# Optimization experiments

Measured on AMD Instinct MI355X. Metric: run time of the kernel, lower is better.

The kernel has to match this reference:

```python
import jax, jax.numpy as jnp
import numpy as np

B, N, D = 32, 1024, 3
Z_SCALES = jnp.array([2.0, 4.0, 8.0, 16.0, 32.0], dtype=jnp.float32)
Z_DIM = 16.0
BETA = 0.01          # kl_warmup done (epoch >= kl_warmup_epochs), so beta == args.beta
SINK_EPS = 0.1       # entropic regularization for the EMD (Sinkhorn) approximation
SINK_ITERS = 20
BIG = 1e8
NEG = -1e9


def _sqdist(x, y):
    # x: [B,N,D], y: [B,M,D] -> squared euclidean distances [B,N,M]
    xx = jnp.sum(x * x, -1)[:, :, None]
    yy = jnp.sum(y * y, -1)[:, None, :]
    xy = jnp.einsum('bnd,bmd->bnm', x, y)
    return jnp.maximum(xx + yy - 2.0 * xy, 0.0)


def _chamfer(x, xm, y, ym):
    # masked bidirectional chamfer: mean over valid points, mean over batch
    d = _sqdist(x, y)                                             # [B,N,M]
    d_xy = jnp.min(jnp.where(ym[:, None, :], d, BIG), axis=2)     # [B,N]
    d_yx = jnp.min(jnp.where(xm[:, :, None], d, BIG), axis=1)     # [B,M]
    nx = jnp.sum(xm, -1).astype(x.dtype)
    ny = jnp.sum(ym, -1).astype(x.dtype)
    cd = (jnp.sum(jnp.where(xm, d_xy, 0.0), -1) / nx
          + jnp.sum(jnp.where(ym, d_yx, 0.0), -1) / ny)
    return jnp.mean(cd)


def _emd_sinkhorn(x, xm, y, ym):
    # entropic-OT approximation of the masked EMD (log-domain Sinkhorn)
    C = _sqdist(x, y)                                             # [B,N,M]
    C = jnp.where(xm[:, :, None] & ym[:, None, :], C, BIG)
    nx = jnp.sum(xm, -1).astype(x.dtype)                          # [B]
    ny = jnp.sum(ym, -1).astype(x.dtype)
    log_a = jnp.where(xm, -jnp.log(nx)[:, None], NEG)             # [B,N]
    log_b = jnp.where(ym, -jnp.log(ny)[:, None], NEG)             # [B,M]

    @jax.checkpoint
    def step(carry, _):
        f, g = carry
        f = SINK_EPS * (log_a - jax.nn.logsumexp((g[:, None, :] - C) / SINK_EPS, axis=2))
        g = SINK_EPS * (log_b - jax.nn.logsumexp((f[:, :, None] - C) / SINK_EPS, axis=1))
        return (f, g), None

    f0 = jnp.zeros_like(log_a)
    g0 = jnp.zeros_like(log_b)
    (f, g), _ = jax.lax.scan(step, (f0, g0), None, length=SINK_ITERS)
    logP = (f[:, :, None] + g[:, None, :] - C) / SINK_EPS         # transport plan (log)
    emd = jnp.sum(jnp.exp(logP) * C, axis=(1, 2))                 # [B]
    return jnp.mean(emd)


def setup_inputs() -> dict:
    key = jax.random.key(0)
    k1, k2, k3 = jax.random.split(key, 3)
    return {
        'output_set': jax.random.normal(k1, (B, N, D), dtype=jnp.float32),
        'output_mask': jnp.ones((B, N), dtype=bool),
        'target_set': jax.random.normal(k2, (B, N, D), dtype=jnp.float32),
        'target_mask': jnp.ones((B, N), dtype=bool),
        'kls': jax.random.uniform(k3, (B, Z_SCALES.shape[0]), dtype=jnp.float32),
    }


def reference(output_set, output_mask, target_set, target_mask, kls):
    cd = _chamfer(output_set, output_mask, target_set, target_mask)
    emd = _emd_sinkhorn(output_set, output_mask, target_set, target_mask)
    recon_loss = cd + emd
    kl_loss = jnp.mean(jnp.sum(kls, axis=1))
    loss = BETA * kl_loss + recon_loss
    topdown_kl = jnp.mean(kls, axis=0) / (Z_SCALES * Z_DIM)        # [L]
    return loss, kl_loss, recon_loss, topdown_kl
```

## Files before the change

kernel.cpp:

```cpp
#include <hip/hip_runtime.h>
#include <math.h>

#define BB 32
#define NN 1024
#define NEGV (-1e9f)
#define BIGC (1e8f)
#define EPSS 0.1f
#define K2f   14.426950408889634f
#define TWOK2 28.853900817779268f
#define INVK2 0.06931471805599453f
#define SINK_ITERS 20
#define CHUNKS 16

__device__ __forceinline__ float wave_reduce_sum(float v) {
#pragma unroll
  for (int s = 32; s >= 1; s >>= 1) v += __shfl_xor(v, s, 64);
  return v;
}
__device__ __forceinline__ float wave_reduce_max(float v) {
#pragma unroll
  for (int s = 32; s >= 1; s >>= 1) v = fmaxf(v, __shfl_xor(v, s, 64));
  return v;
}
__device__ __forceinline__ float wave_reduce_min(float v) {
#pragma unroll
  for (int s = 32; s >= 1; s >>= 1) v = fminf(v, __shfl_xor(v, s, 64));
  return v;
}

__global__ __launch_bounds__(1024) void prep_kernel(
    const float* __restrict__ xset, const int* __restrict__ xm,
    const float* __restrict__ yset, const int* __restrict__ ym,
    float4* __restrict__ xpack, float4* __restrict__ ypack,
    float* __restrict__ elax, float* __restrict__ elay,
    float* __restrict__ invx, float* __restrict__ invy)
{
  const int b = blockIdx.x;
  const int n = threadIdx.x;
  const size_t idx = (size_t)b * NN + n;

  const float x0 = xset[idx * 3 + 0], x1 = xset[idx * 3 + 1], x2 = xset[idx * 3 + 2];
  const float y0 = yset[idx * 3 + 0], y1 = yset[idx * 3 + 1], y2 = yset[idx * 3 + 2];
  xpack[idx] = make_float4(x0, x1, x2, x0 * x0 + x1 * x1 + x2 * x2);
  ypack[idx] = make_float4(y0, y1, y2, y0 * y0 + y1 * y1 + y2 * y2);

  float cx = wave_reduce_sum(xm[idx] ? 1.0f : 0.0f);
  float cy = wave_reduce_sum(ym[idx] ? 1.0f : 0.0f);

  __shared__ float sx[16], sy[16];
  const int wave = n >> 6, lane = n & 63;
  if (lane == 0) { sx[wave] = cx; sy[wave] = cy; }
  __syncthreads();
  if (n == 0) {
    float a = 0.0f, c = 0.0f;
#pragma unroll
    for (int i = 0; i < 16; ++i) { a += sx[i]; c += sy[i]; }
    elax[b] = -EPSS * logf(a);
    elay[b] = -EPSS * logf(c);
    invx[b] = 1.0f / a;
    invy[b] = 1.0f / c;
  }
}

template<bool FIRST, bool CHAMF>
__global__ __launch_bounds__(512) void sink_step(
    const float4* __restrict__ rowpk, const float4* __restrict__ redpk,
    const int* __restrict__ rowmask, const int* __restrict__ redmask,
    const float* __restrict__ pot_in, float* __restrict__ pot_out,
    const float* __restrict__ ela,
    const float* __restrict__ invn,
    float* __restrict__ cd_part)
{
  const int b = blockIdx.y, chunk = blockIdx.x, tid = threadIdx.x;
  const int wave = tid >> 6, lane = tid & 63;
  const size_t base = (size_t)b * NN;

  __shared__ float4 ypk[NN];
  __shared__ float Aj[NN];
  __shared__ float reds[8];

  for (int i = tid; i < NN; i += 512) {
    const float4 yp = redpk[base + i];
    ypk[i] = yp;
    float a;
    if constexpr (FIRST)
      a = redmask[base + i] ? (-K2f * yp.w) : -1e30f;
    else
      a = redmask[base + i] ? fmaf(K2f, pot_in[base + i], -K2f * yp.w) : -1e30f;
    Aj[i] = a;
  }
  __syncthreads();

  const float elab = ela[b];
  float cdacc = 0.0f;

#pragma unroll 1
  for (int grp = 0; grp < 2; ++grp) {
    const int row0 = chunk * 64 + wave * 8 + grp * 4;

    float xs0[4], xs1[4], xs2[4], xw[4];
    int rmv[4];
#pragma unroll
    for (int r = 0; r < 4; ++r) {
      const float4 xp = rowpk[base + row0 + r];
      xs0[r] = TWOK2 * xp.x; xs1[r] = TWOK2 * xp.y; xs2[r] = TWOK2 * xp.z;
      xw[r] = xp.w;
      rmv[r] = rowmask[base + row0 + r];
    }

    float u[4][16];
#pragma unroll
    for (int j = 0; j < 16; ++j) {
      const int m = lane + j * 64;
      const float4 yp = ypk[m];
      const float aj = Aj[m];
#pragma unroll
      for (int r = 0; r < 4; ++r) {
        float t = fmaf(xs0[r], yp.x, aj);
        t = fmaf(xs1[r], yp.y, t);
        t = fmaf(xs2[r], yp.z, t);
        u[r][j] = t;
      }
    }

    float gm[4];
#pragma unroll
    for (int r = 0; r < 4; ++r) {
      const float a0 = fmaxf(fmaxf(u[r][0], u[r][1]), u[r][2]);
      const float a1 = fmaxf(fmaxf(u[r][3], u[r][4]), u[r][5]);
      const float a2 = fmaxf(fmaxf(u[r][6], u[r][7]), u[r][8]);
      const float a3 = fmaxf(fmaxf(u[r][9], u[r][10]), u[r][11]);
      const float a4 = fmaxf(fmaxf(u[r][12], u[r][13]), u[r][14]);
      const float mr = fmaxf(fmaxf(fmaxf(a0, a1), a2),
                             fmaxf(fmaxf(a3, a4), u[r][15]));
      gm[r] = wave_reduce_max(mr);
    }

    float ss[4] = {0.f, 0.f, 0.f, 0.f};
#pragma unroll
    for (int j = 0; j < 16; ++j) {
#pragma unroll
      for (int r = 0; r < 4; ++r)
        ss[r] += __builtin_amdgcn_exp2f(u[r][j] - gm[r]);
    }
#pragma unroll
    for (int r = 0; r < 4; ++r) ss[r] = wave_reduce_sum(ss[r]);

    if (lane == 0) {
#pragma unroll
      for (int r = 0; r < 4; ++r) {
        const float lse2 = gm[r] + __builtin_amdgcn_logf(ss[r]);
        const float el = rmv[r] ? elab : (EPSS * NEGV);
        pot_out[base + row0 + r] = el + xw[r] - INVK2 * lse2;
        if constexpr (CHAMF) {
          if (rmv[r])
            cdacc += fmaxf(fmaf(-INVK2, gm[r], xw[r]), 0.0f);
        }
      }
    }
  }

  if constexpr (CHAMF) {
    if (lane == 0) reds[wave] = cdacc;
    __syncthreads();
    if (tid == 0) {
      float s = 0.f;
#pragma unroll
      for (int w = 0; w < 8; ++w) s += reds[w];
      cd_part[(size_t)b * CHUNKS + chunk] = s * invn[b] * (1.0f / BB);
    }
  }
}

__global__ __launch_bounds__(512) void sink_fast(
    const float4* __restrict__ rowpk, const float4* __restrict__ redpk,
    const int* __restrict__ rowmask, const int* __restrict__ redmask,
    const float* __restrict__ pot_in, float* __restrict__ fpot,
    const float* __restrict__ ela)
{
  const int b = blockIdx.y, chunk = blockIdx.x, tid = threadIdx.x;
  const int wave = tid >> 6, lane = tid & 63;
  const size_t base = (size_t)b * NN;

  __shared__ float4 colq[NN];

  for (int i = tid; i < NN; i += 512) {
    const float4 yp = redpk[base + i];
    const float aj = redmask[base + i]
        ? fmaf(K2f, pot_in[base + i], -K2f * yp.w) : -1e30f;
    colq[i] = make_float4(yp.x, yp.y, yp.z, aj);
  }
  __syncthreads();

  const float elab = ela[b];
  const int row0 = chunk * 64 + wave * 8;

  float xs0[8], xs1[8], xs2[8], sh[8], acc[8], fp[8];
  int rmv[8];
#pragma unroll
  for (int r = 0; r < 8; ++r) {
    const float4 xp = rowpk[base + row0 + r];
    rmv[r] = rowmask[base + row0 + r];
    fp[r] = fpot[base + row0 + r];
    xs0[r] = TWOK2 * xp.x; xs1[r] = TWOK2 * xp.y; xs2[r] = TWOK2 * xp.z;
    sh[r] = rmv[r] ? (K2f * (elab + xp.w - fp[r])) : 3.0e38f;
    acc[r] = 0.0f;
  }

#pragma unroll 4
  for (int j = 0; j < 16; ++j) {
    const float4 q = colq[lane + j * 64];
#pragma unroll
    for (int r = 0; r < 8; ++r) {
      float t = fmaf(xs0[r], q.x, q.w);
      t = fmaf(xs1[r], q.y, t);
      t = fmaf(xs2[r], q.z, t);
      acc[r] += __builtin_amdgcn_exp2f(t - sh[r]);
    }
  }

#pragma unroll
  for (int r = 0; r < 8; ++r) acc[r] = wave_reduce_sum(acc[r]);

  if (lane == 0) {
#pragma unroll
    for (int r = 0; r < 8; ++r) {
      const float l2 = fminf(fmaxf(__builtin_amdgcn_logf(acc[r]), -120.0f), 120.0f);
      fpot[base + row0 + r] = rmv[r] ? (fp[r] - INVK2 * l2) : (EPSS * NEGV);
    }
  }
}

__global__ __launch_bounds__(512) void chamfer_dir(
    const float4* __restrict__ rowpk, const float4* __restrict__ redpk,
    const int* __restrict__ rowmask, const int* __restrict__ redmask,
    const float* __restrict__ invn, float* __restrict__ part)
{
  const int b = blockIdx.y, chunk = blockIdx.x, tid = threadIdx.x;
  const int wave = tid >> 6, lane = tid & 63;
  const size_t base = (size_t)b * NN;

  __shared__ float4 xw4[NN];
  for (int i = tid; i < NN; i += 512) {
    float4 xp = redpk[base + i];
    xp.w = redmask[base + i] ? xp.w : BIGC;
    xw4[i] = xp;
  }
  __syncthreads();

  float acc = 0.0f;
#pragma unroll 1
  for (int rr = 0; rr < 8; ++rr) {
    const int row = chunk * 64 + wave * 8 + rr;
    const float4 yp = rowpk[base + row];
    const float ys0 = -2.f * yp.x, ys1 = -2.f * yp.y, ys2 = -2.f * yp.z;
    float dmin = BIGC;
#pragma unroll
    for (int j = 0; j < 16; ++j) {
      const float4 xq = xw4[lane + j * 64];
      float d = fmaf(ys0, xq.x, xq.w);
      d = fmaf(ys1, xq.y, d);
      d = fmaf(ys2, xq.z, d);
      dmin = fminf(dmin, d);
    }
    dmin = wave_reduce_min(dmin);
    if (lane == 0 && rowmask[base + row]) acc += fmaxf(yp.w + dmin, 0.0f);
  }

  __shared__ float reds[8];
  if (lane == 0) reds[wave] = acc;
  __syncthreads();
  if (tid == 0) {
    float s = 0.f;
#pragma unroll
    for (int w = 0; w < 8; ++w) s += reds[w];
    part[(size_t)b * CHUNKS + chunk] = s * invn[b] * (1.0f / BB);
  }
}

__global__ __launch_bounds__(512) void emd_kernel(
    const float4* __restrict__ rowpk, const float4* __restrict__ redpk,
    const int* __restrict__ rowmask, const int* __restrict__ redmask,
    const float* __restrict__ frow, const float* __restrict__ gred,
    float* __restrict__ part)
{
  const int b = blockIdx.y, chunk = blockIdx.x, tid = threadIdx.x;
  const int wave = tid >> 6, lane = tid & 63;
  const size_t base = (size_t)b * NN;

  __shared__ float4 ypk[NN];
  __shared__ float Ag[NN];
  __shared__ float gv[NN];
  for (int i = tid; i < NN; i += 512) {
    const float4 yp = redpk[base + i];
    ypk[i] = yp;
    const float gg = gred[base + i];
    gv[i] = gg;
    Ag[i] = redmask[base + i] ? fmaf(K2f, gg, -K2f * yp.w) : -1e30f;
  }
  __syncthreads();

  float acc = 0.0f;
#pragma unroll 1
  for (int rr = 0; rr < 8; ++rr) {
    const int row = chunk * 64 + wave * 8 + rr;
    const float4 xp = rowpk[base + row];
    const float fv = frow[base + row];
    const float rc = fmaf(K2f, fv, -K2f * xp.w);
    const float xs0 = TWOK2 * xp.x, xs1 = TWOK2 * xp.y, xs2 = TWOK2 * xp.z;
    const bool rv = rowmask[base + row] != 0;
#pragma unroll
    for (int j = 0; j < 16; ++j) {
      const int m = lane + j * 64;
      const float4 yp = ypk[m];
      const float a = rv ? (Ag[m] + rc) : -1e30f;
      float t = fmaf(xs0, yp.x, a);
      t = fmaf(xs1, yp.y, t);
      t = fmaf(xs2, yp.z, t);
      float C = fmaf(t, -INVK2, fv + gv[m]);
      C = fmaxf(C, 0.0f);
      acc = fmaf(__builtin_amdgcn_exp2f(t), C, acc);
    }
  }

  acc = wave_reduce_sum(acc);
  __shared__ float reds[8];
  if (lane == 0) reds[wave] = acc;
  __syncthreads();
  if (tid == 0) {
    float s = 0.f;
#pragma unroll
    for (int w = 0; w < 8; ++w) s += reds[w];
    part[(size_t)b * CHUNKS + chunk] = s * (1.0f / BB);
  }
}

__global__ __launch_bounds__(256) void final_kernel(
    const float* __restrict__ cd_part, const float* __restrict__ emd_part,
    const float* __restrict__ kls, float* __restrict__ out)
{
  const int tid = threadIdx.x, wave = tid >> 6, lane = tid & 63;
  __shared__ float sh[12];
  float s1 = 0.f, s2 = 0.f, s3 = 0.f;
  for (int i = tid; i < 2 * BB * CHUNKS; i += 256) s1 += cd_part[i];
  for (int i = tid; i < BB * CHUNKS; i += 256) s2 += emd_part[i];
  for (int i = tid; i < BB * 5; i += 256) s3 += kls[i];
  s1 = wave_reduce_sum(s1); s2 = wave_reduce_sum(s2); s3 = wave_reduce_sum(s3);
  if (lane == 0) { sh[wave] = s1; sh[4 + wave] = s2; sh[8 + wave] = s3; }
  __syncthreads();
  if (tid == 0) {
    const float cd = sh[0] + sh[1] + sh[2] + sh[3];
    const float emd = sh[4] + sh[5] + sh[6] + sh[7];
    const float kl = (sh[8] + sh[9] + sh[10] + sh[11]) / (float)BB;
    out[0] = 0.01f * kl + (cd + emd);
    out[1] = kl;
    out[2] = cd + emd;
  }
  if (tid < 5) {
    float cs = 0.f;
    for (int b2 = 0; b2 < BB; ++b2) cs += kls[b2 * 5 + tid];
    const float zs[5] = {2.f, 4.f, 8.f, 16.f, 32.f};
    out[3 + tid] = (cs / (float)BB) / (zs[tid] * 16.f);
  }
}

extern "C" void kernel_launch(void* const* d_in, const int* in_sizes, int n_in,
                              void* d_out, int out_size, void* d_ws, size_t ws_size,
                              hipStream_t stream)
{
  const float* xset = (const float*)d_in[0];
  const int*   xm   = (const int*)d_in[1];
  const float* yset = (const float*)d_in[2];
  const int*   ym   = (const int*)d_in[3];
  const float* kls  = (const float*)d_in[4];

  float* ws = (float*)d_ws;
  float*  f    = ws;
  float*  g    = f + BB * NN;
  float4* xp4  = (float4*)(g + BB * NN);
  float4* yp4  = xp4 + BB * NN;
  float*  elax = (float*)(yp4 + BB * NN);
  float*  elay = elax + BB;
  float*  invx = elay + BB;
  float*  invy = invx + BB;
  float*  cd   = invy + BB;
  float*  emdp = cd + 2 * BB * CHUNKS;

  prep_kernel<<<dim3(BB), 1024, 0, stream>>>(xset, xm, yset, ym,
                                             xp4, yp4, elax, elay, invx, invy);

  const dim3 sg(CHUNKS, BB);
  sink_step<true, true><<<sg, 512, 0, stream>>>(xp4, yp4, xm, ym, nullptr, f,
                                                elax, invx, cd);
  chamfer_dir<<<sg, 512, 0, stream>>>(yp4, xp4, ym, xm, invy, cd + BB * CHUNKS);
  sink_step<false, false><<<sg, 512, 0, stream>>>(yp4, xp4, ym, xm, f, g,
                                                  elay, nullptr, nullptr);
  for (int it = 1; it < SINK_ITERS; ++it) {
    sink_fast<<<sg, 512, 0, stream>>>(xp4, yp4, xm, ym, g, f, elax);
    sink_fast<<<sg, 512, 0, stream>>>(yp4, xp4, ym, xm, f, g, elay);
  }

  emd_kernel<<<sg, 512, 0, stream>>>(xp4, yp4, xm, ym, f, g, emdp);
  final_kernel<<<1, 256, 0, stream>>>(cd, emdp, kls, (float*)d_out);
}
```

Measured before the change: 444.2 us.

## Fuse Sinkhorn iterations into one cooperative kernel with per-batch barriers

Replaces the chain of about 43 kernel launches (prep, chamfer, 40 Sinkhorn half-steps, EMD) with one cooperative persistent kernel of 512 blocks. Each batch's 16 blocks sync through an atomic counter barrier, and point data stays in LDS for the whole run instead of being reloaded on every launch. This removes launch overhead and the repeated global loads of packed points. The cost is spin-wait barriers, a large LDS footprint per block, and reliance on all blocks being co-resident, with a fallback to the old kernel chain if the cooperative launch fails.

```diff
diff --git a/kernel.cpp b/kernel.cpp
--- a/kernel.cpp
+++ b/kernel.cpp
@@ -11,6 +11,7 @@
 #define INVK2 0.06931471805599453f
 #define SINK_ITERS 20
 #define CHUNKS 16
+#define NBLK (BB * CHUNKS)
 
 __device__ __forceinline__ float wave_reduce_sum(float v) {
 #pragma unroll
@@ -26,6 +27,319 @@
 #pragma unroll
   for (int s = 32; s >= 1; s >>= 1) v = fminf(v, __shfl_xor(v, s, 64));
   return v;
+}
+
+__device__ __forceinline__ bool getbit(const unsigned* mb, int i) {
+  return (mb[i >> 5] >> (i & 31)) & 1u;
+}
+
+__device__ __forceinline__ float pot_ld(const float* p) {
+  return __hip_atomic_load(p, __ATOMIC_RELAXED, __HIP_MEMORY_SCOPE_AGENT);
+}
+__device__ __forceinline__ void pot_st(float* p, float v) {
+  __hip_atomic_store(p, v, __ATOMIC_RELAXED, __HIP_MEMORY_SCOPE_AGENT);
+}
+
+__device__ __forceinline__ void batch_barrier(int* bar, int b, int gen, int tid) {
+  __syncthreads();
+  if (tid == 0) {
+    __hip_atomic_fetch_add(&bar[b], 1, __ATOMIC_RELEASE, __HIP_MEMORY_SCOPE_AGENT);
+    const int target = CHUNKS * gen;
+    while (__hip_atomic_load(&bar[b], __ATOMIC_RELAXED, __HIP_MEMORY_SCOPE_AGENT) < target)
+      __builtin_amdgcn_s_sleep(2);
+    (void)__hip_atomic_load(&bar[b], __ATOMIC_ACQUIRE, __HIP_MEMORY_SCOPE_AGENT);
+  }
+  __syncthreads();
+}
+
+template<bool CHAMF>
+__device__ __forceinline__ void twopass(
+    const float4* rl, const float4* cl, const float* Agl, const unsigned* rmb,
+    float elab, int c, int wave, int lane, int tid,
+    float* __restrict__ potOut, size_t base,
+    float invnb, int b, float* __restrict__ cdPart, float* reds)
+{
+  float cdacc = 0.0f;
+#pragma unroll 1
+  for (int grp = 0; grp < 2; ++grp) {
+    const int row0 = c * 64 + wave * 8 + grp * 4;
+
+    float xs0[4], xs1[4], xs2[4], xw[4];
+    bool rmv[4];
+#pragma unroll
+    for (int r = 0; r < 4; ++r) {
+      const float4 xp = rl[row0 + r];
+      xs0[r] = TWOK2 * xp.x; xs1[r] = TWOK2 * xp.y; xs2[r] = TWOK2 * xp.z;
+      xw[r] = xp.w;
+      rmv[r] = getbit(rmb, row0 + r);
+    }
+
+    float u[4][16];
+#pragma unroll
+    for (int j = 0; j < 16; ++j) {
+      const int m = lane + j * 64;
+      const float4 yp = cl[m];
+      const float aj = Agl[m];
+#pragma unroll
+      for (int r = 0; r < 4; ++r) {
+        float t = fmaf(xs0[r], yp.x, aj);
+        t = fmaf(xs1[r], yp.y, t);
+        t = fmaf(xs2[r], yp.z, t);
+        u[r][j] = t;
+      }
+    }
+
+    float gm[4];
+#pragma unroll
+    for (int r = 0; r < 4; ++r) {
+      const float a0 = fmaxf(fmaxf(u[r][0], u[r][1]), u[r][2]);
+      const float a1 = fmaxf(fmaxf(u[r][3], u[r][4]), u[r][5]);
+      const float a2 = fmaxf(fmaxf(u[r][6], u[r][7]), u[r][8]);
+      const float a3 = fmaxf(fmaxf(u[r][9], u[r][10]), u[r][11]);
+      const float a4 = fmaxf(fmaxf(u[r][12], u[r][13]), u[r][14]);
+      const float mr = fmaxf(fmaxf(fmaxf(a0, a1), a2),
+                             fmaxf(fmaxf(a3, a4), u[r][15]));
+      gm[r] = wave_reduce_max(mr);
+    }
+
+    float ss[4] = {0.f, 0.f, 0.f, 0.f};
+#pragma unroll
+    for (int j = 0; j < 16; ++j) {
+#pragma unroll
+      for (int r = 0; r < 4; ++r)
+        ss[r] += __builtin_amdgcn_exp2f(u[r][j] - gm[r]);
+    }
+#pragma unroll
+    for (int r = 0; r < 4; ++r) ss[r] = wave_reduce_sum(ss[r]);
+
+#pragma unroll
+    for (int r = 0; r < 4; ++r) {
+      const float lse2 = gm[r] + __builtin_amdgcn_logf(ss[r]);
+      const float el = rmv[r] ? elab : (EPSS * NEGV);
+      const float pv = el + xw[r] - INVK2 * lse2;
+      if (lane == 0) {
+        pot_st(&potOut[base + row0 + r], pv);
+        if constexpr (CHAMF) {
+          if (rmv[r]) cdacc += fmaxf(fmaf(-INVK2, gm[r], xw[r]), 0.0f);
+        }
+      }
+    }
+  }
+
+  if constexpr (CHAMF) {
+    if (lane == 0) reds[wave] = cdacc;
+    __syncthreads();
+    if (tid == 0) {
+      float s = 0.f;
+#pragma unroll
+      for (int w = 0; w < 8; ++w) s += reds[w];
+      cdPart[(size_t)b * CHUNKS + c] = s * invnb * (1.0f / BB);
+    }
+  }
+}
+
+__device__ __forceinline__ void onepass(
+    const float4* rl, const float4* cl, const float* Agl, const unsigned* rmb,
+    float elab, int row0, int lane, float* __restrict__ pot, size_t base)
+{
+  float xs0[8], xs1[8], xs2[8], sh[8], acc[8], fp[8];
+  bool rmv[8];
+#pragma unroll
+  for (int r = 0; r < 8; ++r) {
+    const float4 xp = rl[row0 + r];
+    rmv[r] = getbit(rmb, row0 + r);
+    fp[r] = pot_ld(&pot[base + row0 + r]);
+    xs0[r] = TWOK2 * xp.x; xs1[r] = TWOK2 * xp.y; xs2[r] = TWOK2 * xp.z;
+    sh[r] = rmv[r] ? (K2f * (elab + xp.w - fp[r])) : 3.0e38f;
+    acc[r] = 0.0f;
+  }
+
+#pragma unroll 4
+  for (int j = 0; j < 16; ++j) {
+    const int m = lane + j * 64;
+    const float4 q = cl[m];
+    const float aj = Agl[m];
+#pragma unroll
+    for (int r = 0; r < 8; ++r) {
+      float t = fmaf(xs0[r], q.x, aj);
+      t = fmaf(xs1[r], q.y, t);
+      t = fmaf(xs2[r], q.z, t);
+      acc[r] += __builtin_amdgcn_exp2f(t - sh[r]);
+    }
+  }
+
+#pragma unroll
+  for (int r = 0; r < 8; ++r) acc[r] = wave_reduce_sum(acc[r]);
+
+  if (lane == 0) {
+#pragma unroll
+    for (int r = 0; r < 8; ++r) {
+      const float l2 = fminf(fmaxf(__builtin_amdgcn_logf(acc[r]), -120.0f), 120.0f);
+      pot_st(&pot[base + row0 + r], rmv[r] ? (fp[r] - INVK2 * l2) : (EPSS * NEGV));
+    }
+  }
+}
+
+__global__ __launch_bounds__(512, 4) void fused_sink(
+    const float* __restrict__ xset, const int* __restrict__ xm,
+    const float* __restrict__ yset, const int* __restrict__ ym,
+    float* __restrict__ f, float* __restrict__ g,
+    float* __restrict__ cd_part, float* __restrict__ emd_part,
+    int* __restrict__ bar)
+{
+  const int gid = blockIdx.x;
+  const int b = gid & (BB - 1), c = gid >> 5;
+  const int tid = threadIdx.x, wave = tid >> 6, lane = tid & 63;
+  const size_t base = (size_t)b * NN;
+
+  __shared__ float4 xl[NN];
+  __shared__ float4 yl[NN];
+  __shared__ float Ag[NN];
+  __shared__ float gvs[NN];
+  __shared__ unsigned xmb[NN / 32], ymb[NN / 32];
+  __shared__ float cred[16];
+  __shared__ float reds[8];
+  __shared__ float sscal[4];
+
+  float cntx = 0.f, cnty = 0.f;
+  for (int i = tid; i < NN; i += 512) {
+    const size_t ix = (base + (size_t)i) * 3;
+    const float x0 = xset[ix], x1 = xset[ix + 1], x2 = xset[ix + 2];
+    const float y0 = yset[ix], y1 = yset[ix + 1], y2 = yset[ix + 2];
+    xl[i] = make_float4(x0, x1, x2, x0 * x0 + x1 * x1 + x2 * x2);
+    yl[i] = make_float4(y0, y1, y2, y0 * y0 + y1 * y1 + y2 * y2);
+    const int mxv = xm[base + i], myv = ym[base + i];
+    cntx += mxv ? 1.0f : 0.0f;
+    cnty += myv ? 1.0f : 0.0f;
+    const unsigned long long bx = __ballot(mxv != 0);
+    const unsigned long long by = __ballot(myv != 0);
+    if (lane == 0) {
+      const int w0 = i >> 5;
+      xmb[w0] = (unsigned)bx; xmb[w0 + 1] = (unsigned)(bx >> 32);
+      ymb[w0] = (unsigned)by; ymb[w0 + 1] = (unsigned)(by >> 32);
+    }
+  }
+  cntx = wave_reduce_sum(cntx);
+  cnty = wave_reduce_sum(cnty);
+  if (lane == 0) { cred[wave] = cntx; cred[8 + wave] = cnty; }
+  __syncthreads();
+  if (tid == 0) {
+    float a = 0.f, cc = 0.f;
+#pragma unroll
+    for (int i = 0; i < 8; ++i) { a += cred[i]; cc += cred[8 + i]; }
+    sscal[0] = -EPSS * logf(a);
+    sscal[1] = -EPSS * logf(cc);
+    sscal[2] = 1.0f / a;
+    sscal[3] = 1.0f / cc;
+  }
+  __syncthreads();
+  const float elax = sscal[0], elay = sscal[1], invx = sscal[2], invy = sscal[3];
+  int gen = 0;
+
+  for (int i = tid; i < NN; i += 512)
+    Ag[i] = getbit(ymb, i) ? (-K2f * yl[i].w) : -1e30f;
+  __syncthreads();
+  twopass<true>(xl, yl, Ag, xmb, elax, c, wave, lane, tid, f, base,
+                invx, b, cd_part, reds);
+
+  for (int i = tid; i < NN; i += 512)
+    gvs[i] = getbit(xmb, i) ? xl[i].w : BIGC;
+  __syncthreads();
+  {
+    float acc = 0.0f;
+#pragma unroll 1
+    for (int rr = 0; rr < 8; ++rr) {
+      const int row = c * 64 + wave * 8 + rr;
+      const float4 yp = yl[row];
+      const float ys0 = -2.f * yp.x, ys1 = -2.f * yp.y, ys2 = -2.f * yp.z;
+      float dmin = BIGC;
+#pragma unroll
+      for (int j = 0; j < 16; ++j) {
+        const int m = lane + j * 64;
+        const float4 xq = xl[m];
+        float d = fmaf(ys0, xq.x, gvs[m]);
+        d = fmaf(ys1, xq.y, d);
+        d = fmaf(ys2, xq.z, d);
+        dmin = fminf(dmin, d);
+      }
+      dmin = wave_reduce_min(dmin);
+      if (lane == 0 && getbit(ymb, row)) acc += fmaxf(yp.w + dmin, 0.0f);
+    }
+    __syncthreads();
+    if (lane == 0) reds[wave] = acc;
+    __syncthreads();
+    if (tid == 0) {
+      float s = 0.f;
+#pragma unroll
+      for (int w = 0; w < 8; ++w) s += reds[w];
+      cd_part[BB * CHUNKS + (size_t)b * CHUNKS + c] = s * invy * (1.0f / BB);
+    }
+  }
+
+  batch_barrier(bar, b, ++gen, tid);
+
+  for (int i = tid; i < NN; i += 512)
+    Ag[i] = getbit(xmb, i) ? fmaf(K2f, pot_ld(&f[base + i]), -K2f * xl[i].w) : -1e30f;
+  __syncthreads();
+  twopass<false>(yl, xl, Ag, ymb, elay, c, wave, lane, tid, g, base,
+                 0.f, b, nullptr, reds);
+
+  batch_barrier(bar, b, ++gen, tid);
+
+  for (int it = 1; it < SINK_ITERS; ++it) {
+    for (int i = tid; i < NN; i += 512)
+      Ag[i] = getbit(ymb, i) ? fmaf(K2f, pot_ld(&g[base + i]), -K2f * yl[i].w) : -1e30f;
+    __syncthreads();
+    onepass(xl, yl, Ag, xmb, elax, c * 64 + wave * 8, lane, f, base);
+    batch_barrier(bar, b, ++gen, tid);
+
+    for (int i = tid; i < NN; i += 512)
+      Ag[i] = getbit(xmb, i) ? fmaf(K2f, pot_ld(&f[base + i]), -K2f * xl[i].w) : -1e30f;
+    __syncthreads();
+    onepass(yl, xl, Ag, ymb, elay, c * 64 + wave * 8, lane, g, base);
+    batch_barrier(bar, b, ++gen, tid);
+  }
+
+  for (int i = tid; i < NN; i += 512) {
+    const float gg = pot_ld(&g[base + i]);
+    gvs[i] = gg;
+    Ag[i] = getbit(ymb, i) ? fmaf(K2f, gg, -K2f * yl[i].w) : -1e30f;
+  }
+  __syncthreads();
+  {
+    float acc = 0.0f;
+#pragma unroll 1
+    for (int rr = 0; rr < 8; ++rr) {
+      const int row = c * 64 + wave * 8 + rr;
+      const float4 xp = xl[row];
+      const float fv = pot_ld(&f[base + row]);
+      const float rc = fmaf(K2f, fv, -K2f * xp.w);
+      const float xs0 = TWOK2 * xp.x, xs1 = TWOK2 * xp.y, xs2 = TWOK2 * xp.z;
+      const bool rv = getbit(xmb, row);
+#pragma unroll
+      for (int j = 0; j < 16; ++j) {
+        const int m = lane + j * 64;
+        const float4 yp = yl[m];
+        const float a = rv ? (Ag[m] + rc) : -1e30f;
+        float t = fmaf(xs0, yp.x, a);
+        t = fmaf(xs1, yp.y, t);
+        t = fmaf(xs2, yp.z, t);
+        float C = fmaf(t, -INVK2, fv + gvs[m]);
+        C = fmaxf(C, 0.0f);
+        acc = fmaf(__builtin_amdgcn_exp2f(t), C, acc);
+      }
+    }
+    acc = wave_reduce_sum(acc);
+    __syncthreads();
+    if (lane == 0) reds[wave] = acc;
+    __syncthreads();
+    if (tid == 0) {
+      float s = 0.f;
+#pragma unroll
+      for (int w = 0; w < 8; ++w) s += reds[w];
+      emd_part[(size_t)b * CHUNKS + c] = s * (1.0f / BB);
+    }
+  }
 }
 
 __global__ __launch_bounds__(1024) void prep_kernel(
@@ -377,29 +691,38 @@
   float* ws = (float*)d_ws;
   float*  f    = ws;
   float*  g    = f + BB * NN;
-  float4* xp4  = (float4*)(g + BB * NN);
-  float4* yp4  = xp4 + BB * NN;
-  float*  elax = (float*)(yp4 + BB * NN);
+  float*  cd   = g + BB * NN;
+  float*  emdp = cd + 2 * BB * CHUNKS;
+  float*  elax = emdp + BB * CHUNKS;
   float*  elay = elax + BB;
   float*  invx = elay + BB;
   float*  invy = invx + BB;
-  float*  cd   = invy + BB;
-  float*  emdp = cd + 2 * BB * CHUNKS;
-
-  prep_kernel<<<dim3(BB), 1024, 0, stream>>>(xset, xm, yset, ym,
-                                             xp4, yp4, elax, elay, invx, invy);
-
-  const dim3 sg(CHUNKS, BB);
-  sink_step<true, true><<<sg, 512, 0, stream>>>(xp4, yp4, xm, ym, nullptr, f,
-                                                elax, invx, cd);
-  chamfer_dir<<<sg, 512, 0, stream>>>(yp4, xp4, ym, xm, invy, cd + BB * CHUNKS);
-  sink_step<false, false><<<sg, 512, 0, stream>>>(yp4, xp4, ym, xm, f, g,
-                                                  elay, nullptr, nullptr);
-  for (int it = 1; it < SINK_ITERS; ++it) {
-    sink_fast<<<sg, 512, 0, stream>>>(xp4, yp4, xm, ym, g, f, elax);
-    sink_fast<<<sg, 512, 0, stream>>>(yp4, xp4, ym, xm, f, g, elay);
-  }
-
-  emd_kernel<<<sg, 512, 0, stream>>>(xp4, yp4, xm, ym, f, g, emdp);
+  int*    bar  = (int*)(invy + BB);
+  float4* xp4  = (float4*)(ws + 67232);
+  float4* yp4  = xp4 + BB * NN;
+
+  hipMemsetAsync(bar, 0, BB * sizeof(int), stream);
+
+  void* args[] = {(void*)&xset, (void*)&xm, (void*)&yset, (void*)&ym,
+                  (void*)&f, (void*)&g, (void*)&cd, (void*)&emdp, (void*)&bar};
+  hipError_t cerr = hipLaunchCooperativeKernel(
+      reinterpret_cast<void*>(fused_sink), dim3(NBLK), dim3(512), args, 0, stream);
+
+  if (cerr != hipSuccess) {
+    prep_kernel<<<dim3(BB), 1024, 0, stream>>>(xset, xm, yset, ym,
+                                               xp4, yp4, elax, elay, invx, invy);
+    const dim3 sg(CHUNKS, BB);
+    sink_step<true, true><<<sg, 512, 0, stream>>>(xp4, yp4, xm, ym, nullptr, f,
+                                                  elax, invx, cd);
+    chamfer_dir<<<sg, 512, 0, stream>>>(yp4, xp4, ym, xm, invy, cd + BB * CHUNKS);
+    sink_step<false, false><<<sg, 512, 0, stream>>>(yp4, xp4, ym, xm, f, g,
+                                                    elay, nullptr, nullptr);
+    for (int it = 1; it < SINK_ITERS; ++it) {
+      sink_fast<<<sg, 512, 0, stream>>>(xp4, yp4, xm, ym, g, f, elax);
+      sink_fast<<<sg, 512, 0, stream>>>(yp4, xp4, ym, xm, f, g, elay);
+    }
+    emd_kernel<<<sg, 512, 0, stream>>>(xp4, yp4, xm, ym, f, g, emdp);
+  }
+
   final_kernel<<<1, 256, 0, stream>>>(cd, emdp, kls, (float*)d_out);
 }
```

After: 1.053 ms. 137% more time.
